# Performance work log

Hardware: AMD Instinct MI355X
Metric: run time of the kernel (lower is better)

## Reference

```python
import jax, jax.numpy as jnp
import numpy as np

N_NODES = 20000
N_EDGES = 256000
DIM = 128
N_LAYERS = 4


def _bn(x, gamma, beta, eps=1e-5):
    # BatchNorm1d in training mode: batch statistics over the node/edge axis
    mu = x.mean(0)
    var = ((x - mu) ** 2).mean(0)
    return gamma * (x - mu) * jax.lax.rsqrt(var + eps) + beta


def setup_inputs() -> dict:
    key = jax.random.key(0)
    ks = jax.random.split(key, 32)
    s = 1.0 / np.sqrt(DIM)
    inp = {
        'h': jax.random.normal(ks[0], (N_NODES, DIM), jnp.float32),
        'e': jax.random.normal(ks[1], (N_EDGES, DIM), jnp.float32),
        'src': jax.random.randint(ks[2], (N_EDGES,), 0, N_NODES, jnp.int32),
        'dst': jax.random.randint(ks[3], (N_EDGES,), 0, N_NODES, jnp.int32),
        'W_emb_h': jax.random.normal(ks[4], (DIM, DIM), jnp.float32) * s,
        'b_emb_h': jnp.zeros((DIM,), jnp.float32),
        'W_emb_e': jax.random.normal(ks[5], (DIM, DIM), jnp.float32) * s,
        'b_emb_e': jnp.zeros((DIM,), jnp.float32),
    }
    for i, nm in enumerate(['A', 'B', 'C', 'D', 'E']):
        inp[nm + 'w'] = jax.random.normal(ks[6 + i], (N_LAYERS, DIM, DIM), jnp.float32) * s
        inp[nm + 'b'] = jnp.zeros((N_LAYERS, DIM), jnp.float32)
    inp['gh'] = jnp.ones((N_LAYERS, DIM), jnp.float32)
    inp['bh'] = jnp.zeros((N_LAYERS, DIM), jnp.float32)
    inp['ge'] = jnp.ones((N_LAYERS, DIM), jnp.float32)
    inp['be'] = jnp.zeros((N_LAYERS, DIM), jnp.float32)
    return inp


def reference(h, e, src, dst, W_emb_h, b_emb_h, W_emb_e, b_emb_e,
              Aw, Ab, Bw, Bb, Cw, Cb, Dw, Db, Ew, Eb, gh, bh, ge, be):
    n_nodes = h.shape[0]
    # input embeddings
    h = h @ W_emb_h + b_emb_h
    e = e @ W_emb_e + b_emb_e
    for l in range(Aw.shape[0]):
        h_in, e_in = h, e
        Ah = h @ Aw[l] + Ab[l]
        Bh = h @ Bw[l] + Bb[l]
        Dh = h @ Dw[l] + Db[l]
        Eh = h @ Ew[l] + Eb[l]
        Ce = e @ Cw[l] + Cb[l]
        # edge gates: e_ij = D h_i + E h_j + C e_ij  (edge i->j)
        e_new = Dh[src] + Eh[dst] + Ce            # [E, D]
        sigma = jax.nn.sigmoid(e_new)
        num = jax.ops.segment_sum(sigma * Bh[src], dst, num_segments=n_nodes)
        den = jax.ops.segment_sum(sigma, dst, num_segments=n_nodes)
        h_new = Ah + num / (den + 1e-6)
        h_new = _bn(h_new, gh[l], bh[l])
        e_new = _bn(e_new, ge[l], be[l])
        # relu + residual (dropout = 0)
        h = h_in + jax.nn.relu(h_new)
        e = e_in + jax.nn.relu(e_new)
    return h
```

## Files before the change

### kernel.cpp

```cpp
#include <hip/hip_runtime.h>
#include <hip/hip_bf16.h>

typedef __attribute__((ext_vector_type(8))) short short8;
typedef __attribute__((ext_vector_type(4))) float floatx4;
typedef __attribute__((ext_vector_type(4))) unsigned short ushortx4;

typedef __attribute__((address_space(3))) unsigned int lds_u32;
typedef __attribute__((address_space(1))) const unsigned int g_u32;

__device__ __forceinline__ float bf2f(unsigned short u) {
    union { float f; unsigned int i; } v; v.i = ((unsigned int)u) << 16; return v.f;
}
__device__ __forceinline__ unsigned short f2bf(float f) {
    union { float f; unsigned int i; } v; v.f = f;
    unsigned int r = v.i + 0x7fffu + ((v.i >> 16) & 1u);
    return (unsigned short)(r >> 16);
}

__global__ void deg_count(const int* __restrict__ dst, int* __restrict__ deg, int E) {
    int i = blockIdx.x * 256 + threadIdx.x;
    if (i < E) atomicAdd(&deg[dst[i]], 1);
}

__global__ __launch_bounds__(1024) void scan_rowptr(const int* __restrict__ deg,
                                                    int* __restrict__ rowptr,
                                                    int* __restrict__ cursor, int N) {
    const int CH = 20;
    __shared__ int buf[1024];
    int t = threadIdx.x;
    int base = t * CH;
    int local[CH];
    int tot = 0;
#pragma unroll
    for (int k = 0; k < CH; ++k) {
        int i = base + k;
        int v = (i < N) ? deg[i] : 0;
        local[k] = tot;
        tot += v;
    }
    buf[t] = tot;
    __syncthreads();
    for (int off = 1; off < 1024; off <<= 1) {
        int x = (t >= off) ? buf[t - off] : 0;
        __syncthreads();
        buf[t] += x;
        __syncthreads();
    }
    int excl = buf[t] - tot;
#pragma unroll
    for (int k = 0; k < CH; ++k) {
        int i = base + k;
        if (i < N) { rowptr[i] = excl + local[k]; cursor[i] = excl + local[k]; }
    }
    if (t == 1023) rowptr[N] = buf[1023];
}

__global__ void scatter_edges(const int* __restrict__ src, const int* __restrict__ dst,
                              int* __restrict__ cursor, int* __restrict__ eix,
                              int* __restrict__ sx, int* __restrict__ dstx, int E) {
    int i = blockIdx.x * 256 + threadIdx.x;
    if (i >= E) return;
    int d = dst[i];
    int pos = atomicAdd(&cursor[d], 1);
    eix[pos] = i;
    sx[pos] = src[i];
    dstx[pos] = d;
}

__global__ void transpose_w(const float* __restrict__ Wh,
                            const float* __restrict__ We,
                            const float* __restrict__ Aw,
                            const float* __restrict__ Bw,
                            const float* __restrict__ Cw,
                            const float* __restrict__ Dw,
                            const float* __restrict__ Ew,
                            unsigned short* __restrict__ Wt) {
    int i = blockIdx.x * 256 + threadIdx.x;
    const int total = 22 * 16384;
    if (i >= total) return;
    int slot = i >> 14;
    int r = i & 16383;
    int n = r >> 7;
    int k = r & 127;
    const float* srcp;
    if (slot == 0) srcp = Wh;
    else if (slot == 1) srcp = We;
    else {
        int t = slot - 2;
        int l = t / 5, w = t % 5;
        const float* bases[5] = {Aw, Bw, Cw, Dw, Ew};
        srcp = bases[w] + l * 16384;
    }
    Wt[i] = f2bf(srcp[k * 128 + n]);
}

template <int IN_F32, int OUT_BF16, int GATHER>
__global__ __launch_bounds__(256) void gemm_lds(const void* __restrict__ Ain,
                                                const int* __restrict__ ridx,
                                                const unsigned short* __restrict__ Wt,
                                                const float* __restrict__ bias,
                                                void* __restrict__ Cout,
                                                int nTiles, int Mrows) {
    constexpr int ROWB = IN_F32 ? 512 : 256;
    constexpr int RSH = IN_F32 ? 9 : 8;
    constexpr int TILEB = 64 * ROWB;
    constexpr int PERW = TILEB / 4;
    constexpr int ROUNDS = PERW / 1024;
    __shared__ unsigned char smem[2][TILEB];

    const int lane = threadIdx.x & 63;
    const int wv = threadIdx.x >> 6;
    const int m16 = lane & 15;
    const int kg = lane >> 4;

    short8 b[4][2];
#pragma unroll
    for (int j = 0; j < 2; ++j)
#pragma unroll
        for (int ks = 0; ks < 4; ++ks)
            b[ks][j] = *(const short8*)(Wt + ((wv * 2 + j) * 16 + m16) * 128 + ks * 32 + kg * 8);
    floatx4 bv[2];
#pragma unroll
    for (int j = 0; j < 2; ++j)
        bv[j] = *(const floatx4*)(bias + (wv * 2 + j) * 16 + kg * 4);

    const unsigned char* Ab = (const unsigned char*)Ain;

    int t0 = blockIdx.x;
    if (t0 >= nTiles) return;

    auto stage = [&](int bufsel, int t) {
#pragma unroll
        for (int r = 0; r < ROUNDS; ++r) {
            int d = wv * PERW + r * 1024 + lane * 16;
            int row = d >> RSH;
            int scol;
            if (IN_F32)
                scol = (d ^ ((row & 3) << 5)) & (ROWB - 1);
            else
                scol = (d ^ ((row & 7) << 4)) & (ROWB - 1);
            int grow = t * 64 + row;
            grow = grow < Mrows ? grow : Mrows - 1;
            if (GATHER) grow = ridx[grow];
            const unsigned char* gp = Ab + (size_t)grow * ROWB + scol;
            unsigned char* lp = &smem[bufsel][wv * PERW + r * 1024];
            __builtin_amdgcn_global_load_lds((g_u32*)gp, (lds_u32*)lp, 16, 0, 0);
        }
    };

    int cur = 0;
    stage(0, t0);
    __syncthreads();

    for (int t = t0; t < nTiles; t += gridDim.x) {
        int tn = t + gridDim.x;
        if (tn < nTiles) stage(cur ^ 1, tn);

        const unsigned char* sb = smem[cur];
#pragma unroll
        for (int st = 0; st < 4; ++st) {
            short8 a[4];
#pragma unroll
            for (int ks = 0; ks < 4; ++ks) {
                if (IN_F32) {
                    int aoff = (st * 16 + m16) * 512 + ks * 128 + kg * 32;
                    aoff ^= (m16 & 3) << 5;
                    floatx4 f0 = *(const floatx4*)(sb + aoff);
                    floatx4 f1 = *(const floatx4*)(sb + aoff + 16);
                    short8 tt;
                    tt[0] = (short)f2bf(f0[0]); tt[1] = (short)f2bf(f0[1]);
                    tt[2] = (short)f2bf(f0[2]); tt[3] = (short)f2bf(f0[3]);
                    tt[4] = (short)f2bf(f1[0]); tt[5] = (short)f2bf(f1[1]);
                    tt[6] = (short)f2bf(f1[2]); tt[7] = (short)f2bf(f1[3]);
                    a[ks] = tt;
                } else {
                    int aoff = (st * 16 + m16) * 256 + ks * 64 + kg * 16;
                    aoff ^= (m16 & 7) << 4;
                    a[ks] = *(const short8*)(sb + aoff);
                }
            }
            floatx4 acc0 = (floatx4){0.f, 0.f, 0.f, 0.f};
            floatx4 acc1 = (floatx4){0.f, 0.f, 0.f, 0.f};
#pragma unroll
            for (int ks = 0; ks < 4; ++ks) {
                acc0 = __builtin_amdgcn_mfma_f32_16x16x32_bf16(b[ks][0], a[ks], acc0, 0, 0, 0);
                acc1 = __builtin_amdgcn_mfma_f32_16x16x32_bf16(b[ks][1], a[ks], acc1, 0, 0, 0);
            }
            size_t row = (size_t)t * 64 + st * 16 + m16;
#pragma unroll
            for (int j = 0; j < 2; ++j) {
                int c0 = (wv * 2 + j) * 16 + kg * 4;
                floatx4 accj = j ? acc1 : acc0;
                if (OUT_BF16) {
                    ushortx4 o;
#pragma unroll
                    for (int i = 0; i < 4; ++i) o[i] = f2bf(accj[i] + bv[j][i]);
                    *(ushortx4*)((unsigned short*)Cout + row * 128 + c0) = o;
                } else {
                    floatx4 o;
#pragma unroll
                    for (int i = 0; i < 4; ++i) o[i] = accj[i] + bv[j][i];
                    *(floatx4*)((float*)Cout + row * 128 + c0) = o;
                }
            }
        }
        __syncthreads();
        cur ^= 1;
    }
}

__global__ __launch_bounds__(1024) void gemm_h4(const float* __restrict__ h_cur,
                                                const unsigned short* __restrict__ WtL,
                                                const float* __restrict__ Abi,
                                                const float* __restrict__ Bbi,
                                                const float* __restrict__ Dbi,
                                                const float* __restrict__ Ebi,
                                                float* __restrict__ AhB,
                                                unsigned short* __restrict__ BD16,
                                                unsigned short* __restrict__ Eh16,
                                                int nStrips) {
    const int lane = threadIdx.x & 63;
    const int w = threadIdx.x >> 6;
    const int m16 = lane & 15;
    const int kg = lane >> 4;

    short8 bf[4][2];
    floatx4 bv[2];
    if (w < 8) {
        const int slot = (w < 4) ? 0 : 4;
        const float* bp = (w < 4) ? Abi : Ebi;
        const int ntb = (w & 3) * 2;
#pragma unroll
        for (int j = 0; j < 2; ++j) {
#pragma unroll
            for (int ks = 0; ks < 4; ++ks)
                bf[ks][j] = *(const short8*)(WtL + slot * 16384 +
                                             ((ntb + j) * 16 + m16) * 128 + ks * 32 + kg * 8);
            bv[j] = *(const floatx4*)(bp + (ntb + j) * 16 + kg * 4);
        }
    } else {
        const int nt = w - 8;
#pragma unroll
        for (int ks = 0; ks < 4; ++ks) {
            bf[ks][0] = *(const short8*)(WtL + 1 * 16384 + (nt * 16 + m16) * 128 + ks * 32 + kg * 8);
            bf[ks][1] = *(const short8*)(WtL + 3 * 16384 + (nt * 16 + m16) * 128 + ks * 32 + kg * 8);
        }
        bv[0] = *(const floatx4*)(Bbi + nt * 16 + kg * 4);
        bv[1] = *(const floatx4*)(Dbi + nt * 16 + kg * 4);
    }

    for (int s = blockIdx.x; s < nStrips; s += gridDim.x) {
        size_t rowBase = ((size_t)s * 16 + m16) * 128;
        short8 a[4];
#pragma unroll
        for (int ks = 0; ks < 4; ++ks) {
            int off = ks * 32 + kg * 8;
            floatx4 f0 = *(const floatx4*)(h_cur + rowBase + off);
            floatx4 f1 = *(const floatx4*)(h_cur + rowBase + off + 4);
            short8 t;
            t[0] = (short)f2bf(f0[0]); t[1] = (short)f2bf(f0[1]);
            t[2] = (short)f2bf(f0[2]); t[3] = (short)f2bf(f0[3]);
            t[4] = (short)f2bf(f1[0]); t[5] = (short)f2bf(f1[1]);
            t[6] = (short)f2bf(f1[2]); t[7] = (short)f2bf(f1[3]);
            a[ks] = t;
        }

        floatx4 acc0 = (floatx4){0.f, 0.f, 0.f, 0.f};
        floatx4 acc1 = (floatx4){0.f, 0.f, 0.f, 0.f};
#pragma unroll
        for (int ks = 0; ks < 4; ++ks) {
            acc0 = __builtin_amdgcn_mfma_f32_16x16x32_bf16(bf[ks][0], a[ks], acc0, 0, 0, 0);
            acc1 = __builtin_amdgcn_mfma_f32_16x16x32_bf16(bf[ks][1], a[ks], acc1, 0, 0, 0);
        }

        size_t r = (size_t)s * 16 + m16;
        if (w < 4) {
            const int ntb = (w & 3) * 2;
            floatx4 o0, o1;
#pragma unroll
            for (int i = 0; i < 4; ++i) { o0[i] = acc0[i] + bv[0][i]; o1[i] = acc1[i] + bv[1][i]; }
            *(floatx4*)(AhB + r * 128 + (ntb + 0) * 16 + kg * 4) = o0;
            *(floatx4*)(AhB + r * 128 + (ntb + 1) * 16 + kg * 4) = o1;
        } else if (w < 8) {
            const int ntb = (w & 3) * 2;
            ushortx4 o0, o1;
#pragma unroll
            for (int i = 0; i < 4; ++i) {
                o0[i] = f2bf(acc0[i] + bv[0][i]);
                o1[i] = f2bf(acc1[i] + bv[1][i]);
            }
            *(ushortx4*)(Eh16 + r * 128 + (ntb + 0) * 16 + kg * 4) = o0;
            *(ushortx4*)(Eh16 + r * 128 + (ntb + 1) * 16 + kg * 4) = o1;
        } else {
            const int nt = w - 8;
            short8 o;
#pragma unroll
            for (int i = 0; i < 4; ++i) {
                o[2 * i]     = (short)f2bf(acc0[i] + bv[0][i]);
                o[2 * i + 1] = (short)f2bf(acc1[i] + bv[1][i]);
            }
            *(short8*)(BD16 + r * 256 + (nt * 16 + kg * 4) * 2) = o;
        }
    }
}

template <int DO_E>
__global__ __launch_bounds__(256) void node_aggregate(const unsigned short* __restrict__ Ce,
                                                      const unsigned short* __restrict__ BD16,
                                                      const unsigned short* __restrict__ Eh16,
                                                      const int* __restrict__ rowptr,
                                                      const int* __restrict__ sx,
                                                      const float* __restrict__ Ah,
                                                      float* __restrict__ h_new,
                                                      float* __restrict__ sums, int N) {
    const int q = threadIdx.x & 31;
    const int g = threadIdx.x >> 5;
    float hs[4] = {0.f, 0.f, 0.f, 0.f};
    float hq[4] = {0.f, 0.f, 0.f, 0.f};
    float es[4] = {0.f, 0.f, 0.f, 0.f};
    float eq[4] = {0.f, 0.f, 0.f, 0.f};
    for (int d = blockIdx.x * 8 + g; d < N; d += gridDim.x * 8) {
        int beg = rowptr[d], end = rowptr[d + 1];
        ushortx4 eh4 = *(const ushortx4*)(Eh16 + (size_t)d * 128 + q * 4);
        float ehf[4];
#pragma unroll
        for (int k = 0; k < 4; ++k) ehf[k] = bf2f(eh4[k]);
        float num[4] = {0.f, 0.f, 0.f, 0.f};
        float den[4] = {0.f, 0.f, 0.f, 0.f};
        int j = beg;
        for (; j + 1 < end; j += 2) {
            int s0 = sx[j], s1 = sx[j + 1];
            ushortx4 c0 = *(const ushortx4*)(Ce + (size_t)j * 128 + q * 4);
            ushortx4 c1 = *(const ushortx4*)(Ce + (size_t)(j + 1) * 128 + q * 4);
            short8 bd0 = *(const short8*)(BD16 + (size_t)s0 * 256 + q * 8);
            short8 bd1 = *(const short8*)(BD16 + (size_t)s1 * 256 + q * 8);
#pragma unroll
            for (int k = 0; k < 4; ++k) {
                float en0 = bf2f(c0[k]) + bf2f((unsigned short)bd0[2 * k + 1]) + ehf[k];
                float en1 = bf2f(c1[k]) + bf2f((unsigned short)bd1[2 * k + 1]) + ehf[k];
                if (DO_E) {
                    es[k] += en0 + en1;
                    eq[k] += en0 * en0 + en1 * en1;
                }
                float sg0 = __builtin_amdgcn_rcpf(1.f + __expf(-en0));
                float sg1 = __builtin_amdgcn_rcpf(1.f + __expf(-en1));
                den[k] += sg0 + sg1;
                num[k] += sg0 * bf2f((unsigned short)bd0[2 * k])
                        + sg1 * bf2f((unsigned short)bd1[2 * k]);
            }
        }
        if (j < end) {
            int s0 = sx[j];
            ushortx4 c0 = *(const ushortx4*)(Ce + (size_t)j * 128 + q * 4);
            short8 bd0 = *(const short8*)(BD16 + (size_t)s0 * 256 + q * 8);
#pragma unroll
            for (int k = 0; k < 4; ++k) {
                float en0 = bf2f(c0[k]) + bf2f((unsigned short)bd0[2 * k + 1]) + ehf[k];
                if (DO_E) {
                    es[k] += en0;
                    eq[k] += en0 * en0;
                }
                float sg0 = __builtin_amdgcn_rcpf(1.f + __expf(-en0));
                den[k] += sg0;
                num[k] += sg0 * bf2f((unsigned short)bd0[2 * k]);
            }
        }
        floatx4 ah = *(const floatx4*)(Ah + (size_t)d * 128 + q * 4);
        floatx4 out;
#pragma unroll
        for (int k = 0; k < 4; ++k) {
            float v = ah[k] + num[k] / (den[k] + 1e-6f);
            out[k] = v;
            hs[k] += v;
            hq[k] += v * v;
        }
        *(floatx4*)(h_new + (size_t)d * 128 + q * 4) = out;
    }
    __shared__ float ls[512];
    ls[threadIdx.x] = 0.f;
    ls[256 + threadIdx.x] = 0.f;
    __syncthreads();
#pragma unroll
    for (int k = 0; k < 4; ++k) {
        atomicAdd(&ls[q * 4 + k], hs[k]);
        atomicAdd(&ls[128 + q * 4 + k], hq[k]);
        if (DO_E) {
            atomicAdd(&ls[256 + q * 4 + k], es[k]);
            atomicAdd(&ls[384 + q * 4 + k], eq[k]);
        }
    }
    __syncthreads();
    atomicAdd(&sums[threadIdx.x], ls[threadIdx.x]);
    if (DO_E) atomicAdd(&sums[256 + threadIdx.x], ls[256 + threadIdx.x]);
}

__global__ void finalize_stats(const float* __restrict__ sums,
                               const float* __restrict__ gh,
                               const float* __restrict__ bh,
                               const float* __restrict__ ge,
                               const float* __restrict__ be,
                               float* __restrict__ coef, int N, int E) {
    int c = threadIdx.x;
    if (c >= 128) return;
    float muh = sums[c] / (float)N;
    float vh = fmaxf(sums[128 + c] / (float)N - muh * muh, 0.f);
    float rsh = rsqrtf(vh + 1e-5f);
    float g = gh[c], bt = bh[c];
    coef[c] = g * rsh;
    coef[128 + c] = bt - g * rsh * muh;
    float mue = sums[256 + c] / (float)E;
    float ve = fmaxf(sums[384 + c] / (float)E - mue * mue, 0.f);
    float rse = rsqrtf(ve + 1e-5f);
    float g2 = ge[c], b2 = be[c];
    coef[256 + c] = g2 * rse;
    coef[384 + c] = b2 - g2 * rse * mue;
}

__global__ __launch_bounds__(256) void h_update(const float* __restrict__ h_new,
                                                const float* __restrict__ coef,
                                                float* __restrict__ h_cur,
                                                float* __restrict__ out, int N) {
    const int c = threadIdx.x & 127;
    float sa = coef[c], sb = coef[128 + c];
    int total = N * 128;
    for (int i = blockIdx.x * blockDim.x + threadIdx.x; i < total; i += gridDim.x * blockDim.x) {
        float v = h_new[i] * sa + sb;
        v = v > 0.f ? v : 0.f;
        float h = h_cur[i] + v;
        h_cur[i] = h;
        if (out) out[i] = h;
    }
}

__global__ __launch_bounds__(256) void e_update(const unsigned short* __restrict__ Ce,
                                                const unsigned short* __restrict__ BD16,
                                                const unsigned short* __restrict__ Eh16,
                                                const int* __restrict__ sx,
                                                const int* __restrict__ dstx,
                                                const float* __restrict__ coef,
                                                unsigned short* __restrict__ e_cur, int E) {
    int total8 = E * 16;
    for (int idx = blockIdx.x * blockDim.x + threadIdx.x; idx < total8;
         idx += gridDim.x * blockDim.x) {
        int j = idx >> 4;
        int c8 = (idx & 15) * 8;
        int sr = sx[j], dr = dstx[j];
        short8 ce = *(const short8*)(Ce + (size_t)idx * 8);
        short8 ec = *(const short8*)(e_cur + (size_t)idx * 8);
        short8 eh = *(const short8*)(Eh16 + (size_t)dr * 128 + c8);
        short8 bd0 = *(const short8*)(BD16 + (size_t)sr * 256 + c8 * 2);
        short8 bd1 = *(const short8*)(BD16 + (size_t)sr * 256 + c8 * 2 + 8);
        floatx4 sa0 = *(const floatx4*)(coef + 256 + c8);
        floatx4 sa1 = *(const floatx4*)(coef + 256 + c8 + 4);
        floatx4 sb0 = *(const floatx4*)(coef + 384 + c8);
        floatx4 sb1 = *(const floatx4*)(coef + 384 + c8 + 4);
        short8 r;
#pragma unroll
        for (int k = 0; k < 8; ++k) {
            unsigned short dh = (unsigned short)((k < 4) ? bd0[2 * k + 1] : bd1[2 * (k - 4) + 1]);
            float en = bf2f((unsigned short)ce[k]) + bf2f(dh) + bf2f((unsigned short)eh[k]);
            float sa = (k < 4) ? sa0[k] : sa1[k - 4];
            float sb = (k < 4) ? sb0[k] : sb1[k - 4];
            float v = en * sa + sb;
            v = v > 0.f ? v : 0.f;
            r[k] = (short)f2bf(bf2f((unsigned short)ec[k]) + v);
        }
        *(short8*)(e_cur + (size_t)idx * 8) = r;
    }
}

extern "C" void kernel_launch(void* const* d_in, const int* in_sizes, int n_in,
                              void* d_out, int out_size, void* d_ws, size_t ws_size,
                              hipStream_t stream) {
    const int N = 20000, E = 256000, L = 4;
    const int NPAD = 20032;

    const float* h_in = (const float*)d_in[0];
    const float* e_in = (const float*)d_in[1];
    const int* src = (const int*)d_in[2];
    const int* dst = (const int*)d_in[3];
    const float* Wemb_h = (const float*)d_in[4];
    const float* bemb_h = (const float*)d_in[5];
    const float* Wemb_e = (const float*)d_in[6];
    const float* bemb_e = (const float*)d_in[7];
    const float* Aw = (const float*)d_in[8];
    const float* Abi = (const float*)d_in[9];
    const float* Bw = (const float*)d_in[10];
    const float* Bbi = (const float*)d_in[11];
    const float* Cw = (const float*)d_in[12];
    const float* Cbi = (const float*)d_in[13];
    const float* Dw = (const float*)d_in[14];
    const float* Dbi = (const float*)d_in[15];
    const float* Ew = (const float*)d_in[16];
    const float* Ebi = (const float*)d_in[17];
    const float* gh = (const float*)d_in[18];
    const float* bh = (const float*)d_in[19];
    const float* ge = (const float*)d_in[20];
    const float* be = (const float*)d_in[21];

    char* p = (char*)d_ws;
    auto carve = [&](size_t bytes) {
        void* r = (void*)p;
        p += ((bytes + 255) & ~(size_t)255);
        return r;
    };
    unsigned short* Wt = (unsigned short*)carve((size_t)22 * 16384 * 2);
    float* h_cur = (float*)carve((size_t)NPAD * 128 * 4);
    unsigned short* e_cur = (unsigned short*)carve((size_t)E * 128 * 2);
    unsigned short* e_new = (unsigned short*)carve((size_t)E * 128 * 2);
    float* AhB = (float*)carve((size_t)N * 128 * 4);
    unsigned short* BD16 = (unsigned short*)carve((size_t)N * 256 * 2);
    unsigned short* Eh16 = (unsigned short*)carve((size_t)N * 128 * 2);
    float* h_newB = (float*)carve((size_t)N * 128 * 4);
    float* sums = (float*)carve(4 * 128 * 4);
    float* coef = (float*)carve(4 * 128 * 4);
    int* deg = (int*)carve((size_t)N * 4);
    int* rowptr = (int*)carve((size_t)(N + 1) * 4);
    int* cursor = (int*)carve((size_t)N * 4);
    int* eix = (int*)carve((size_t)E * 4);
    int* sx = (int*)carve((size_t)E * 4);
    int* dstx = (int*)carve((size_t)E * 4);

    hipMemsetAsync(deg, 0, (size_t)N * 4, stream);
    deg_count<<<(E + 255) / 256, 256, 0, stream>>>(dst, deg, E);
    scan_rowptr<<<1, 1024, 0, stream>>>(deg, rowptr, cursor, N);
    scatter_edges<<<(E + 255) / 256, 256, 0, stream>>>(src, dst, cursor, eix, sx, dstx, E);

    transpose_w<<<(22 * 16384 + 255) / 256, 256, 0, stream>>>(Wemb_h, Wemb_e, Aw, Bw, Cw, Dw, Ew, Wt);

    gemm_lds<1, 0, 0><<<313, 256, 0, stream>>>(h_in, nullptr, Wt + 0 * 16384, bemb_h,
                                               h_cur, 313, N);
    gemm_lds<1, 1, 1><<<1024, 256, 0, stream>>>(e_in, eix, Wt + 1 * 16384, bemb_e,
                                                e_cur, E / 64, E);

    for (int l = 0; l < L; ++l) {
        int last = (l == L - 1);
        hipMemsetAsync(sums, 0, 4 * 128 * 4, stream);
        const unsigned short* WtL = Wt + (size_t)(2 + l * 5) * 16384;
        gemm_h4<<<250, 1024, 0, stream>>>(h_cur, WtL, Abi + l * 128, Bbi + l * 128,
                                          Dbi + l * 128, Ebi + l * 128, AhB, BD16, Eh16,
                                          N / 16);
        gemm_lds<0, 1, 0><<<1024, 256, 0, stream>>>(e_cur, nullptr, WtL + 2 * 16384,
                                                    Cbi + l * 128, e_new, E / 64, E);
        if (!last)
            node_aggregate<1><<<1250, 256, 0, stream>>>(e_new, BD16, Eh16, rowptr, sx, AhB,
                                                        h_newB, sums, N);
        else
            node_aggregate<0><<<1250, 256, 0, stream>>>(e_new, BD16, Eh16, rowptr, sx, AhB,
                                                        h_newB, sums, N);
        finalize_stats<<<1, 128, 0, stream>>>(sums, gh + l * 128, bh + l * 128, ge + l * 128,
                                              be + l * 128, coef, N, E);
        h_update<<<512, 256, 0, stream>>>(h_newB, coef, h_cur, last ? (float*)d_out : nullptr, N);
        if (!last) e_update<<<2048, 256, 0, stream>>>(e_new, BD16, Eh16, sx, dstx, coef,
                                                      e_cur, E);
    }
}
```

Before: 960.1 us.

## Shrink fp32 GEMM tiles, raise grid sizes, unroll edge aggregation by four

Result: slower. 1.002 ms (+4.3%).

```diff
diff --git a/kernel.cpp b/kernel.cpp
--- a/kernel.cpp
+++ b/kernel.cpp
@@ -103,7 +103,8 @@
                                                 int nTiles, int Mrows) {
     constexpr int ROWB = IN_F32 ? 512 : 256;
     constexpr int RSH = IN_F32 ? 9 : 8;
-    constexpr int TILEB = 64 * ROWB;
+    constexpr int ROWS = IN_F32 ? 32 : 64;
+    constexpr int TILEB = ROWS * ROWB;
     constexpr int PERW = TILEB / 4;
     constexpr int ROUNDS = PERW / 1024;
     __shared__ unsigned char smem[2][TILEB];
@@ -139,7 +140,7 @@
                 scol = (d ^ ((row & 3) << 5)) & (ROWB - 1);
             else
                 scol = (d ^ ((row & 7) << 4)) & (ROWB - 1);
-            int grow = t * 64 + row;
+            int grow = t * ROWS + row;
             grow = grow < Mrows ? grow : Mrows - 1;
             if (GATHER) grow = ridx[grow];
             const unsigned char* gp = Ab + (size_t)grow * ROWB + scol;
@@ -158,7 +159,7 @@
 
         const unsigned char* sb = smem[cur];
 #pragma unroll
-        for (int st = 0; st < 4; ++st) {
+        for (int st = 0; st < ROWS / 16; ++st) {
             short8 a[4];
 #pragma unroll
             for (int ks = 0; ks < 4; ++ks) {
@@ -186,7 +187,7 @@
                 acc0 = __builtin_amdgcn_mfma_f32_16x16x32_bf16(b[ks][0], a[ks], acc0, 0, 0, 0);
                 acc1 = __builtin_amdgcn_mfma_f32_16x16x32_bf16(b[ks][1], a[ks], acc1, 0, 0, 0);
             }
-            size_t row = (size_t)t * 64 + st * 16 + m16;
+            size_t row = (size_t)t * ROWS + st * 16 + m16;
 #pragma unroll
             for (int j = 0; j < 2; ++j) {
                 int c0 = (wv * 2 + j) * 16 + kg * 4;
@@ -328,28 +329,31 @@
         float num[4] = {0.f, 0.f, 0.f, 0.f};
         float den[4] = {0.f, 0.f, 0.f, 0.f};
         int j = beg;
-        for (; j + 1 < end; j += 2) {
-            int s0 = sx[j], s1 = sx[j + 1];
-            ushortx4 c0 = *(const ushortx4*)(Ce + (size_t)j * 128 + q * 4);
-            ushortx4 c1 = *(const ushortx4*)(Ce + (size_t)(j + 1) * 128 + q * 4);
-            short8 bd0 = *(const short8*)(BD16 + (size_t)s0 * 256 + q * 8);
-            short8 bd1 = *(const short8*)(BD16 + (size_t)s1 * 256 + q * 8);
-#pragma unroll
-            for (int k = 0; k < 4; ++k) {
-                float en0 = bf2f(c0[k]) + bf2f((unsigned short)bd0[2 * k + 1]) + ehf[k];
-                float en1 = bf2f(c1[k]) + bf2f((unsigned short)bd1[2 * k + 1]) + ehf[k];
-                if (DO_E) {
-                    es[k] += en0 + en1;
-                    eq[k] += en0 * en0 + en1 * en1;
+        for (; j + 3 < end; j += 4) {
+            int sv[4];
+#pragma unroll
+            for (int u = 0; u < 4; ++u) sv[u] = sx[j + u];
+            ushortx4 c[4];
+#pragma unroll
+            for (int u = 0; u < 4; ++u)
+                c[u] = *(const ushortx4*)(Ce + (size_t)(j + u) * 128 + q * 4);
+            short8 bd[4];
+#pragma unroll
+            for (int u = 0; u < 4; ++u)
+                bd[u] = *(const short8*)(BD16 + (size_t)sv[u] * 256 + q * 8);
+#pragma unroll
+            for (int u = 0; u < 4; ++u) {
+#pragma unroll
+                for (int k = 0; k < 4; ++k) {
+                    float en = bf2f(c[u][k]) + bf2f((unsigned short)bd[u][2 * k + 1]) + ehf[k];
+                    if (DO_E) { es[k] += en; eq[k] += en * en; }
+                    float sg = __builtin_amdgcn_rcpf(1.f + __expf(-en));
+                    den[k] += sg;
+                    num[k] += sg * bf2f((unsigned short)bd[u][2 * k]);
                 }
-                float sg0 = __builtin_amdgcn_rcpf(1.f + __expf(-en0));
-                float sg1 = __builtin_amdgcn_rcpf(1.f + __expf(-en1));
-                den[k] += sg0 + sg1;
-                num[k] += sg0 * bf2f((unsigned short)bd0[2 * k])
-                        + sg1 * bf2f((unsigned short)bd1[2 * k]);
-            }
-        }
-        if (j < end) {
+            }
+        }
+        for (; j < end; ++j) {
             int s0 = sx[j];
             ushortx4 c0 = *(const ushortx4*)(Ce + (size_t)j * 128 + q * 4);
             short8 bd0 = *(const short8*)(BD16 + (size_t)s0 * 256 + q * 8);
@@ -473,7 +477,6 @@
                               void* d_out, int out_size, void* d_ws, size_t ws_size,
                               hipStream_t stream) {
     const int N = 20000, E = 256000, L = 4;
-    const int NPAD = 20032;
 
     const float* h_in = (const float*)d_in[0];
     const float* e_in = (const float*)d_in[1];
@@ -505,7 +508,7 @@
         return r;
     };
     unsigned short* Wt = (unsigned short*)carve((size_t)22 * 16384 * 2);
-    float* h_cur = (float*)carve((size_t)NPAD * 128 * 4);
+    float* h_cur = (float*)carve((size_t)N * 128 * 4);
     unsigned short* e_cur = (unsigned short*)carve((size_t)E * 128 * 2);
     unsigned short* e_new = (unsigned short*)carve((size_t)E * 128 * 2);
     float* AhB = (float*)carve((size_t)N * 128 * 4);
@@ -528,10 +531,10 @@
 
     transpose_w<<<(22 * 16384 + 255) / 256, 256, 0, stream>>>(Wemb_h, Wemb_e, Aw, Bw, Cw, Dw, Ew, Wt);
 
-    gemm_lds<1, 0, 0><<<313, 256, 0, stream>>>(h_in, nullptr, Wt + 0 * 16384, bemb_h,
-                                               h_cur, 313, N);
-    gemm_lds<1, 1, 1><<<1024, 256, 0, stream>>>(e_in, eix, Wt + 1 * 16384, bemb_e,
-                                                e_cur, E / 64, E);
+    gemm_lds<1, 0, 0><<<625, 256, 0, stream>>>(h_in, nullptr, Wt + 0 * 16384, bemb_h,
+                                               h_cur, 625, N);
+    gemm_lds<1, 1, 1><<<2000, 256, 0, stream>>>(e_in, eix, Wt + 1 * 16384, bemb_e,
+                                                e_cur, 8000, E);
 
     for (int l = 0; l < L; ++l) {
         int last = (l == L - 1);
@@ -540,7 +543,7 @@
         gemm_h4<<<250, 1024, 0, stream>>>(h_cur, WtL, Abi + l * 128, Bbi + l * 128,
                                           Dbi + l * 128, Ebi + l * 128, AhB, BD16, Eh16,
                                           N / 16);
-        gemm_lds<0, 1, 0><<<1024, 256, 0, stream>>>(e_cur, nullptr, WtL + 2 * 16384,
+        gemm_lds<0, 1, 0><<<2000, 256, 0, stream>>>(e_cur, nullptr, WtL + 2 * 16384,
                                                     Cbi + l * 128, e_new, E / 64, E);
         if (!last)
             node_aggregate<1><<<1250, 256, 0, stream>>>(e_new, BD16, Eh16, rowptr, sx, AhB,
```
